# Kernel optimization log

Hardware: AMD Instinct MI355X
Metric: run time of the kernel (lower is better)

## Reference

```python
import jax, jax.numpy as jnp
import numpy as np

N_NODES = 50000
N_EDGES = 800000
IN_CH = 128
HID = 64
HEADS = 4
OUT_CH = 10
NUM_GRAPHS = 500
NEG_SLOPE = 0.2  # PyG GATConv default LeakyReLU slope


def gat_conv(x, src, dst, W, a_src, a_dst, b, concat):
    """One PyG-style GATConv (inference; attention dropout disabled).
    x: [N, F_in], src/dst: [E'] (self-loops already appended).
    W: [F_in, H*C], a_src/a_dst: [H, C], b: [H*C] or [C].
    """
    N = x.shape[0]
    H, C = a_src.shape
    h = (x @ W).reshape(N, H, C)                      # [N,H,C]
    al_s = jnp.einsum('nhc,hc->nh', h, a_src)          # [N,H]
    al_d = jnp.einsum('nhc,hc->nh', h, a_dst)          # [N,H]
    e = al_s[src] + al_d[dst]                          # [E,H]
    e = jnp.where(e > 0, e, NEG_SLOPE * e)             # leaky_relu
    # segment softmax over edges sharing the same destination node
    e_max = jax.ops.segment_max(e, dst, num_segments=N)
    ex = jnp.exp(e - e_max[dst])
    denom = jax.ops.segment_sum(ex, dst, num_segments=N)
    alpha = ex / (denom[dst] + 1e-16)                  # [E,H]
    msg = h[src] * alpha[:, :, None]                   # [E,H,C]
    out = jax.ops.segment_sum(msg, dst, num_segments=N)  # [N,H,C]
    out = out.reshape(N, H * C) if concat else out.mean(axis=1)
    return out + b


def _forward(x, edge_index, batch, W1, a_src1, a_dst1, b1,
             W2, a_src2, a_dst2, b2, fc_w, fc_b):
    N = x.shape[0]
    loops = jnp.arange(N, dtype=edge_index.dtype)
    src = jnp.concatenate([edge_index[0], loops])
    dst = jnp.concatenate([edge_index[1], loops])
    h = gat_conv(x, src, dst, W1, a_src1, a_dst1, b1, concat=True)
    h = jax.nn.relu(h)                                  # dropout: eval mode
    h = gat_conv(h, src, dst, W2, a_src2, a_dst2, b2, concat=False)
    pooled = jax.ops.segment_sum(h, batch, num_segments=NUM_GRAPHS)  # global_add_pool
    logits = pooled @ fc_w + fc_b
    return jax.nn.log_softmax(logits, axis=1)


def setup_inputs() -> dict:
    key = jax.random.key(0)
    ks = jax.random.split(key, 12)
    g = lambda k, shp, fan: jax.random.normal(k, shp, dtype=jnp.float32) * (1.0 / np.sqrt(fan))
    x = jax.random.normal(ks[0], (N_NODES, IN_CH), dtype=jnp.float32)
    edge_index = jax.random.randint(ks[1], (2, N_EDGES), 0, N_NODES, dtype=jnp.int64)
    batch = jnp.sort(jax.random.randint(ks[2], (N_NODES,), 0, NUM_GRAPHS, dtype=jnp.int64))
    return {
        'x': x,
        'edge_index': edge_index,
        'batch': batch,
        'W1': g(ks[3], (IN_CH, HEADS * HID), IN_CH),
        'a_src1': g(ks[4], (HEADS, HID), HID),
        'a_dst1': g(ks[5], (HEADS, HID), HID),
        'b1': jnp.zeros((HEADS * HID,), dtype=jnp.float32),
        'W2': g(ks[6], (HEADS * HID, HID), HEADS * HID),
        'a_src2': g(ks[7], (1, HID), HID),
        'a_dst2': g(ks[8], (1, HID), HID),
        'b2': jnp.zeros((HID,), dtype=jnp.float32),
        'fc_w': g(ks[9], (HID, OUT_CH), HID),
        'fc_b': jnp.zeros((OUT_CH,), dtype=jnp.float32),
    }


def reference(x, edge_index, batch, W1, a_src1, a_dst1, b1,
              W2, a_src2, a_dst2, b2, fc_w, fc_b):
    return _forward(x, edge_index, batch, W1, a_src1, a_dst1, b1,
                    W2, a_src2, a_dst2, b2, fc_w, fc_b)
```

## Files before the change

kernel.cpp:

```cpp
#include <hip/hip_runtime.h>
#include <hip/hip_fp16.h>
#include <math.h>

#define N_NODES   50000
#define N_EDGES   800000
#define IN_CH     128
#define HID       64
#define HEADS     4
#define F1        (HEADS * HID)
#define OUT_CH    10
#define NUM_GRAPHS 500
#define NEG_SLOPE 0.2f
#define RPAD      132
#define NTILES    (N_NODES / 16)
#define CAP       64

typedef __attribute__((ext_vector_type(8))) _Float16 half8;
typedef __attribute__((ext_vector_type(4))) float floatx4;

__device__ __forceinline__ unsigned short f2h(float f) {
    _Float16 h = (_Float16)f;
    unsigned short u; __builtin_memcpy(&u, &h, 2); return u;
}
__device__ __forceinline__ unsigned int pack_h2(float lo, float hi) {
    auto r = __builtin_amdgcn_cvt_pkrtz(lo, hi);
    unsigned int u; __builtin_memcpy(&u, &r, 4); return u;
}
__device__ __forceinline__ float h2f(unsigned short u) {
    _Float16 h; __builtin_memcpy(&h, &u, 2); return (float)h;
}

__global__ void init_kernel(int* __restrict__ cnt, unsigned short* __restrict__ csr,
                            const float* __restrict__ W1, unsigned short* __restrict__ W1p,
                            const float* __restrict__ W2, unsigned short* __restrict__ W2p)
{
    const int gid = blockIdx.x * blockDim.x + threadIdx.x;
    if (gid < N_NODES) {
        cnt[gid] = 1;
        csr[gid * CAP] = (unsigned short)gid;
    }
    if (gid < 4096) {
        const int t = gid >> 8, kt = (gid >> 6) & 3, l = gid & 63;
        const int col = t * 16 + (l & 15);
        unsigned short* o = W1p + (size_t)((t * 4 + kt) * 64 + l) * 8;
        #pragma unroll
        for (int j = 0; j < 8; ++j) {
            const int k = kt * 32 + (l >> 4) * 8 + j;
            o[j] = f2h(W1[k * F1 + col]);
        }
    } else if (gid < 6144) {
        const int g2 = gid - 4096;
        const int t = g2 >> 9, kt = (g2 >> 6) & 7, l = g2 & 63;
        const int col = t * 16 + (l & 15);
        unsigned short* o = W2p + (size_t)((t * 8 + kt) * 64 + l) * 8;
        #pragma unroll
        for (int j = 0; j < 8; ++j) {
            const int k = kt * 32 + (l >> 4) * 8 + j;
            o[j] = f2h(W2[k * HID + col]);
        }
    }
}

__global__ __launch_bounds__(256) void scatter_gemm1(
    const int* __restrict__ ei, int* __restrict__ cnt,
    unsigned short* __restrict__ csr,
    const float* __restrict__ x, const unsigned short* __restrict__ W1p,
    const float* __restrict__ a_src1, const float* __restrict__ a_dst1,
    unsigned short* __restrict__ H1b,
    float* __restrict__ al_s1, float* __restrict__ al_d1)
{
    const int e = blockIdx.x * 256 + threadIdx.x;
    const int src = ei[e];
    const int dst = ei[N_EDGES + e];
    const int slot = atomicAdd(&cnt[dst], 1);

    const int m0 = blockIdx.x * 16;
    const int w = threadIdx.x >> 6;
    const int l = threadIdx.x & 63;
    const int q = l >> 4, r = l & 15;
    floatx4 acc[4] = {};
    const float* arow = x + (size_t)(m0 + r) * IN_CH + q * 8;
    #pragma unroll
    for (int kt = 0; kt < 4; ++kt) {
        const float4 f0 = *(const float4*)(arow + kt * 32);
        const float4 f1 = *(const float4*)(arow + kt * 32 + 4);
        union { uint4 u; half8 h; } a;
        a.u = make_uint4(pack_h2(f0.x, f0.y), pack_h2(f0.z, f0.w),
                         pack_h2(f1.x, f1.y), pack_h2(f1.z, f1.w));
        #pragma unroll
        for (int t = 0; t < 4; ++t) {
            const int nt = w * 4 + t;
            const half8 b = *(const half8*)(W1p + (size_t)((nt * 4 + kt) * 64 + l) * 8);
            acc[t] = __builtin_amdgcn_mfma_f32_16x16x32_f16(a.h, b, acc[t], 0, 0, 0);
        }
    }
    float ls[4] = {0.f, 0.f, 0.f, 0.f}, ld[4] = {0.f, 0.f, 0.f, 0.f};
    #pragma unroll
    for (int t = 0; t < 4; ++t) {
        const int col = (w * 4 + t) * 16 + r;
        const float as = a_src1[col], ad = a_dst1[col];
        #pragma unroll
        for (int reg = 0; reg < 4; ++reg) {
            H1b[(size_t)(m0 + q * 4 + reg) * F1 + col] = f2h(acc[t][reg]);
            ls[reg] += acc[t][reg] * as;
            ld[reg] += acc[t][reg] * ad;
        }
    }
    #pragma unroll
    for (int reg = 0; reg < 4; ++reg) {
        #pragma unroll
        for (int off = 8; off > 0; off >>= 1) {
            ls[reg] += __shfl_down(ls[reg], off, 16);
            ld[reg] += __shfl_down(ld[reg], off, 16);
        }
    }
    if (r == 0) {
        #pragma unroll
        for (int reg = 0; reg < 4; ++reg) {
            const int n = m0 + q * 4 + reg;
            al_s1[n * HEADS + w] = ls[reg];
            al_d1[n * HEADS + w] = ld[reg];
        }
    }

    if (slot < CAP) csr[dst * CAP + slot] = (unsigned short)src;
}

__global__ __launch_bounds__(256) void agg1_gemm2(
    const int* __restrict__ cnt, const unsigned short* __restrict__ csr,
    const float* __restrict__ al_s1, const float* __restrict__ al_d1,
    const uint2* __restrict__ H1b2, const float* __restrict__ b1,
    const unsigned short* __restrict__ W2p,
    const float* __restrict__ a_src2, const float* __restrict__ a_dst2,
    unsigned short* __restrict__ H2b,
    float* __restrict__ al_s2, float* __restrict__ al_d2)
{
    const int m0 = blockIdx.x * 16;
    const int w = threadIdx.x >> 6;
    const int l = threadIdx.x & 63;
    __shared__ unsigned int rows[16][RPAD];
    __shared__ unsigned int sofs[16][CAP];
    __shared__ float        wts[16][CAP][4];

    int nreg[4];
    #pragma unroll
    for (int d = 0; d < 4; ++d) {
        const int dd = w * 4 + d;
        const int dstn = m0 + dd;
        const int n = min(cnt[dstn], CAP);
        nreg[d] = n;
        const float4 ad = *(const float4*)(al_d1 + dstn * 4);
        float w0 = 0.f, w1 = 0.f, w2 = 0.f, w3 = 0.f;
        unsigned int off = 0;
        if (l < n) {
            const int s = csr[dstn * CAP + l];
            off = (unsigned int)s << 9;
            const float4 as = *(const float4*)(al_s1 + s * 4);
            float t0 = as.x + ad.x; t0 = t0 > 0.f ? t0 : NEG_SLOPE * t0;
            float t1 = as.y + ad.y; t1 = t1 > 0.f ? t1 : NEG_SLOPE * t1;
            float t2 = as.z + ad.z; t2 = t2 > 0.f ? t2 : NEG_SLOPE * t2;
            float t3 = as.w + ad.w; t3 = t3 > 0.f ? t3 : NEG_SLOPE * t3;
            w0 = __expf(t0); w1 = __expf(t1); w2 = __expf(t2); w3 = __expf(t3);
        }
        sofs[dd][l] = off;
        *(float4*)wts[dd][l] = make_float4(w0, w1, w2, w3);
    }
    __syncthreads();

    const int h = l >> 4;
    const unsigned int lane8 = (unsigned int)(l * 8);
    #pragma unroll 1
    for (int d = 0; d < 4; ++d) {
        const int dd = w * 4 + d;
        const int n = nreg[d];
        float a0 = 0.f, a1 = 0.f, a2 = 0.f, a3 = 0.f, den = 0.f;
        const int n4 = (n + 3) & ~3;
        for (int i = 0; i < n4; i += 4) {
            unsigned int off[4]; float wt[4];
            #pragma unroll
            for (int j = 0; j < 4; ++j) {
                off[j] = sofs[dd][i + j];
                wt[j]  = wts[dd][i + j][h];
            }
            uint2 u[4];
            #pragma unroll
            for (int j = 0; j < 4; ++j)
                u[j] = *(const uint2*)((const char*)H1b2 + (off[j] + lane8));
            #pragma unroll
            for (int j = 0; j < 4; ++j) {
                union { uint2 v; _Float16 hv[4]; } c; c.v = u[j];
                a0 += wt[j] * (float)c.hv[0];
                a1 += wt[j] * (float)c.hv[1];
                a2 += wt[j] * (float)c.hv[2];
                a3 += wt[j] * (float)c.hv[3];
                den += wt[j];
            }
        }
        const float rcp = 1.f / (den + 1e-16f);
        const float4 bb = *(const float4*)(b1 + 4 * l);
        float v0 = a0 * rcp + bb.x; v0 = v0 > 0.f ? v0 : 0.f;
        float v1 = a1 * rcp + bb.y; v1 = v1 > 0.f ? v1 : 0.f;
        float v2 = a2 * rcp + bb.z; v2 = v2 > 0.f ? v2 : 0.f;
        float v3 = a3 * rcp + bb.w; v3 = v3 > 0.f ? v3 : 0.f;
        *(uint2*)&rows[dd][2 * l] = make_uint2(pack_h2(v0, v1), pack_h2(v2, v3));
    }
    __syncthreads();

    const int q = l >> 4, r = l & 15;
    floatx4 acc = {};
    #pragma unroll
    for (int kt = 0; kt < 8; ++kt) {
        union { uint4 u; half8 hh; } a;
        a.u = *(const uint4*)&rows[r][kt * 16 + q * 4];
        const half8 b = *(const half8*)(W2p + (size_t)((w * 8 + kt) * 64 + l) * 8);
        acc = __builtin_amdgcn_mfma_f32_16x16x32_f16(a.hh, b, acc, 0, 0, 0);
    }
    const int col = w * 16 + r;
    const float as = a_src2[col], ad2 = a_dst2[col];
    float ls[4], ld[4];
    #pragma unroll
    for (int reg = 0; reg < 4; ++reg) {
        H2b[(size_t)(m0 + q * 4 + reg) * HID + col] = f2h(acc[reg]);
        ls[reg] = acc[reg] * as;
        ld[reg] = acc[reg] * ad2;
    }
    #pragma unroll
    for (int reg = 0; reg < 4; ++reg) {
        #pragma unroll
        for (int off = 8; off > 0; off >>= 1) {
            ls[reg] += __shfl_down(ls[reg], off, 16);
            ld[reg] += __shfl_down(ld[reg], off, 16);
        }
    }
    __shared__ float Ls[4][16], Ld[4][16];
    if (r == 0) {
        #pragma unroll
        for (int reg = 0; reg < 4; ++reg) {
            Ls[w][q * 4 + reg] = ls[reg];
            Ld[w][q * 4 + reg] = ld[reg];
        }
    }
    __syncthreads();
    if (threadIdx.x < 16) {
        const int row = threadIdx.x;
        al_s2[m0 + row] = Ls[0][row] + Ls[1][row] + Ls[2][row] + Ls[3][row];
        al_d2[m0 + row] = Ld[0][row] + Ld[1][row] + Ld[2][row] + Ld[3][row];
    }
}

__global__ __launch_bounds__(256) void agg2_csr(
    const int* __restrict__ cnt, const unsigned short* __restrict__ csr,
    const float* __restrict__ al_s2, const float* __restrict__ al_d2,
    const uint2* __restrict__ H2b2, uint2* __restrict__ out2b)
{
    const int dst = blockIdx.x * 4 + (threadIdx.x >> 6);
    const int l = threadIdx.x & 63;
    const int qt = l >> 4, j = l & 15;
    const int n = min(cnt[dst], CAP);
    const float ad = al_d2[dst];
    float a0 = 0.f, a1 = 0.f, a2 = 0.f, a3 = 0.f, den = 0.f;
    int s_reg = 0;
    float w_reg = 0.f;
    if (l < n) {
        s_reg = csr[dst * CAP + l];
        float t = al_s2[s_reg] + ad;
        t = t > 0.f ? t : NEG_SLOPE * t;
        w_reg = __expf(t);
    }
    const int n8 = (n + 7) & ~7;
    for (int i = 0; i < n8; i += 8) {
        const int e0 = i + qt, e1 = i + 4 + qt;
        const int   src0 = __shfl(s_reg, e0, 64), src1 = __shfl(s_reg, e1, 64);
        const float wt0  = __shfl(w_reg, e0, 64), wt1  = __shfl(w_reg, e1, 64);
        const uint2 u0 = H2b2[(size_t)src0 * (HID / 4) + j];
        const uint2 u1 = H2b2[(size_t)src1 * (HID / 4) + j];
        union { uint2 v; _Float16 hv[4]; } c0, c1; c0.v = u0; c1.v = u1;
        a0 += wt0 * (float)c0.hv[0] + wt1 * (float)c1.hv[0];
        a1 += wt0 * (float)c0.hv[1] + wt1 * (float)c1.hv[1];
        a2 += wt0 * (float)c0.hv[2] + wt1 * (float)c1.hv[2];
        a3 += wt0 * (float)c0.hv[3] + wt1 * (float)c1.hv[3];
        den += wt0 + wt1;
    }
    #pragma unroll
    for (int m = 16; m <= 32; m <<= 1) {
        a0 += __shfl_xor(a0, m, 64);
        a1 += __shfl_xor(a1, m, 64);
        a2 += __shfl_xor(a2, m, 64);
        a3 += __shfl_xor(a3, m, 64);
        den += __shfl_xor(den, m, 64);
    }
    if (l < 16) {
        const float rcp = 1.f / (den + 1e-16f);
        out2b[(size_t)dst * (HID / 4) + j] =
            make_uint2(pack_h2(a0 * rcp, a1 * rcp), pack_h2(a2 * rcp, a3 * rcp));
    }
}

__global__ __launch_bounds__(256) void pool_fc_kernel(
    const unsigned short* __restrict__ out2b, const float* __restrict__ b2,
    const int* __restrict__ batch,
    const float* __restrict__ fc_w, const float* __restrict__ fc_b,
    float* __restrict__ out)
{
    const int g = blockIdx.x;
    const int q = threadIdx.x >> 6, c = threadIdx.x & 63;
    __shared__ int se[2];
    __shared__ float partial[4][HID];
    __shared__ float pl[HID];
    __shared__ float logits[OUT_CH];
    if (threadIdx.x < 2) {
        const int target = g + threadIdx.x;
        int lo = 0, hi = N_NODES;
        while (lo < hi) { int mid = (lo + hi) >> 1; if (batch[mid] < target) lo = mid + 1; else hi = mid; }
        se[threadIdx.x] = lo;
    }
    __syncthreads();
    const int start = se[0], end = se[1];
    float acc = 0.f;
    for (int n = start + q; n < end; n += 4)
        acc += h2f(out2b[(size_t)n * HID + c]);
    partial[q][c] = acc;
    __syncthreads();
    if (q == 0)
        pl[c] = partial[0][c] + partial[1][c] + partial[2][c] + partial[3][c]
              + (float)(end - start) * b2[c];
    __syncthreads();
    if (threadIdx.x < OUT_CH) {
        float lg = fc_b[threadIdx.x];
        #pragma unroll
        for (int k = 0; k < HID; ++k) lg += pl[k] * fc_w[k * OUT_CH + threadIdx.x];
        logits[threadIdx.x] = lg;
    }
    __syncthreads();
    if (threadIdx.x == 0) {
        float m = logits[0];
        #pragma unroll
        for (int j2 = 1; j2 < OUT_CH; ++j2) m = fmaxf(m, logits[j2]);
        float s = 0.f;
        #pragma unroll
        for (int j2 = 0; j2 < OUT_CH; ++j2) s += __expf(logits[j2] - m);
        const float lse = m + __logf(s);
        #pragma unroll
        for (int j2 = 0; j2 < OUT_CH; ++j2) out[g * OUT_CH + j2] = logits[j2] - lse;
    }
}


extern "C" void kernel_launch(void* const* d_in, const int* in_sizes, int n_in,
                              void* d_out, int out_size, void* d_ws, size_t ws_size,
                              hipStream_t stream)
{
    const float* x      = (const float*)d_in[0];
    const int*   ei     = (const int*)  d_in[1];
    const int*   batch  = (const int*)  d_in[2];
    const float* W1     = (const float*)d_in[3];
    const float* a_src1 = (const float*)d_in[4];
    const float* a_dst1 = (const float*)d_in[5];
    const float* b1     = (const float*)d_in[6];
    const float* W2     = (const float*)d_in[7];
    const float* a_src2 = (const float*)d_in[8];
    const float* a_dst2 = (const float*)d_in[9];
    const float* b2     = (const float*)d_in[10];
    const float* fc_w   = (const float*)d_in[11];
    const float* fc_b   = (const float*)d_in[12];
    float* out = (float*)d_out;

    char* ws = (char*)d_ws;
    size_t off = 0;
    auto alloc_b = [&](size_t bytes) { void* p = (void*)(ws + off); off += (bytes + 15) & ~15ull; return p; };

    unsigned short* H1b  = (unsigned short*)alloc_b((size_t)N_NODES * F1 * 2);
    float* al_s1  = (float*)alloc_b((size_t)N_NODES * HEADS * 4);
    float* al_d1  = (float*)alloc_b((size_t)N_NODES * HEADS * 4);
    unsigned short* H2b  = (unsigned short*)alloc_b((size_t)N_NODES * HID * 2);
    float* al_s2  = (float*)alloc_b((size_t)N_NODES * 4);
    float* al_d2  = (float*)alloc_b((size_t)N_NODES * 4);
    unsigned short* out2b = (unsigned short*)alloc_b((size_t)N_NODES * HID * 2);
    int*   cnt    = (int*)alloc_b((size_t)N_NODES * 4);
    unsigned short* csr = (unsigned short*)alloc_b((size_t)N_NODES * CAP * 2);
    unsigned short* W1p = (unsigned short*)alloc_b((size_t)IN_CH * F1 * 2);
    unsigned short* W2p = (unsigned short*)alloc_b((size_t)F1 * HID * 2);

    init_kernel<<<(N_NODES + 255) / 256, 256, 0, stream>>>(cnt, csr, W1, W1p, W2, W2p);

    scatter_gemm1<<<NTILES, 256, 0, stream>>>(ei, cnt, csr, x, W1p,
                                              a_src1, a_dst1, H1b, al_s1, al_d1);

    agg1_gemm2<<<N_NODES / 16, 256, 0, stream>>>(cnt, csr, al_s1, al_d1,
                                                 (const uint2*)H1b, b1,
                                                 W2p, a_src2, a_dst2,
                                                 H2b, al_s2, al_d2);

    agg2_csr<<<N_NODES / 4, 256, 0, stream>>>(cnt, csr, al_s2, al_d2,
                                              (const uint2*)H2b, (uint2*)out2b);

    pool_fc_kernel<<<NUM_GRAPHS, 256, 0, stream>>>(out2b, b2, batch, fc_w, fc_b, out);
}
```

Measured before the change: 240.0 us.

## Store layer-1 features as FP8 e4m3 and gather 16 channels per lane

The layer-1 hidden features H1 are now stored as FP8 e4m3 instead of FP16, which halves the bytes moved by the random-access neighbor gather in agg1_gemm2. The gather is reorganized so each lane loads 16 FP8 channels (uint4) and the four 16-lane groups each process different edges, followed by cross-group shuffle reductions. Attention weights are packed into FP16 in shared memory. The risks are accuracy loss from 8-bit feature storage, extra conversion ALU work and more registers per thread.

Result: no change. 243.0 us (+1.2%).

```diff
diff --git a/kernel.cpp b/kernel.cpp
--- a/kernel.cpp
+++ b/kernel.cpp
@@ -1,5 +1,6 @@
 #include <hip/hip_runtime.h>
 #include <hip/hip_fp16.h>
+#include <hip/hip_fp8.h>
 #include <math.h>
 
 #define N_NODES   50000
@@ -29,6 +30,13 @@
 __device__ __forceinline__ float h2f(unsigned short u) {
     _Float16 h; __builtin_memcpy(&h, &u, 2); return (float)h;
 }
+__device__ __forceinline__ unsigned char f2q(float f) {
+    __hip_fp8_e4m3 q(f);
+    unsigned char u; __builtin_memcpy(&u, &q, 1); return u;
+}
+__device__ __forceinline__ float q2f(unsigned char u) {
+    __hip_fp8_e4m3 q; __builtin_memcpy(&q, &u, 1); return (float)q;
+}
 
 __global__ void init_kernel(int* __restrict__ cnt, unsigned short* __restrict__ csr,
                             const float* __restrict__ W1, unsigned short* __restrict__ W1p,
@@ -66,7 +74,7 @@
     unsigned short* __restrict__ csr,
     const float* __restrict__ x, const unsigned short* __restrict__ W1p,
     const float* __restrict__ a_src1, const float* __restrict__ a_dst1,
-    unsigned short* __restrict__ H1b,
+    unsigned char* __restrict__ H1q,
     float* __restrict__ al_s1, float* __restrict__ al_d1)
 {
     const int e = blockIdx.x * 256 + threadIdx.x;
@@ -101,7 +109,7 @@
         const float as = a_src1[col], ad = a_dst1[col];
         #pragma unroll
         for (int reg = 0; reg < 4; ++reg) {
-            H1b[(size_t)(m0 + q * 4 + reg) * F1 + col] = f2h(acc[t][reg]);
+            H1q[(size_t)(m0 + q * 4 + reg) * F1 + col] = f2q(acc[t][reg]);
             ls[reg] += acc[t][reg] * as;
             ld[reg] += acc[t][reg] * ad;
         }
@@ -129,7 +137,7 @@
 __global__ __launch_bounds__(256) void agg1_gemm2(
     const int* __restrict__ cnt, const unsigned short* __restrict__ csr,
     const float* __restrict__ al_s1, const float* __restrict__ al_d1,
-    const uint2* __restrict__ H1b2, const float* __restrict__ b1,
+    const unsigned char* __restrict__ H1q, const float* __restrict__ b1,
     const unsigned short* __restrict__ W2p,
     const float* __restrict__ a_src2, const float* __restrict__ a_dst2,
     unsigned short* __restrict__ H2b,
@@ -138,9 +146,10 @@
     const int m0 = blockIdx.x * 16;
     const int w = threadIdx.x >> 6;
     const int l = threadIdx.x & 63;
+    const char* H1base = (const char*)H1q;
     __shared__ unsigned int rows[16][RPAD];
     __shared__ unsigned int sofs[16][CAP];
-    __shared__ float        wts[16][CAP][4];
+    __shared__ uint2        wtp[16][CAP];
 
     int nreg[4];
     #pragma unroll
@@ -154,7 +163,7 @@
         unsigned int off = 0;
         if (l < n) {
             const int s = csr[dstn * CAP + l];
-            off = (unsigned int)s << 9;
+            off = (unsigned int)s << 8;
             const float4 as = *(const float4*)(al_s1 + s * 4);
             float t0 = as.x + ad.x; t0 = t0 > 0.f ? t0 : NEG_SLOPE * t0;
             float t1 = as.y + ad.y; t1 = t1 > 0.f ? t1 : NEG_SLOPE * t1;
@@ -163,46 +172,64 @@
             w0 = __expf(t0); w1 = __expf(t1); w2 = __expf(t2); w3 = __expf(t3);
         }
         sofs[dd][l] = off;
-        *(float4*)wts[dd][l] = make_float4(w0, w1, w2, w3);
-    }
-    __syncthreads();
-
-    const int h = l >> 4;
-    const unsigned int lane8 = (unsigned int)(l * 8);
+        wtp[dd][l] = make_uint2(pack_h2(w0, w1), pack_h2(w2, w3));
+    }
+    __syncthreads();
+
+    const int qe = l >> 4;
+    const int j  = l & 15;
+    const int hd = j >> 2;
+    const unsigned int lane16 = (unsigned int)(j * 16);
     #pragma unroll 1
     for (int d = 0; d < 4; ++d) {
         const int dd = w * 4 + d;
         const int n = nreg[d];
-        float a0 = 0.f, a1 = 0.f, a2 = 0.f, a3 = 0.f, den = 0.f;
-        const int n4 = (n + 3) & ~3;
-        for (int i = 0; i < n4; i += 4) {
+        float A[16] = {};
+        float den = 0.f;
+        const int n16 = (n + 15) & ~15;
+        for (int i = 0; i < n16; i += 16) {
             unsigned int off[4]; float wt[4];
             #pragma unroll
-            for (int j = 0; j < 4; ++j) {
-                off[j] = sofs[dd][i + j];
-                wt[j]  = wts[dd][i + j][h];
+            for (int k = 0; k < 4; ++k) {
+                const int slot = i + 4 * k + qe;
+                off[k] = sofs[dd][slot];
+                const uint2 wp = wtp[dd][slot];
+                const unsigned int uw = (hd & 2) ? wp.y : wp.x;
+                wt[k] = h2f((hd & 1) ? (unsigned short)(uw >> 16)
+                                     : (unsigned short)(uw & 0xFFFFu));
             }
-            uint2 u[4];
+            uint4 u[4];
             #pragma unroll
-            for (int j = 0; j < 4; ++j)
-                u[j] = *(const uint2*)((const char*)H1b2 + (off[j] + lane8));
+            for (int k = 0; k < 4; ++k)
+                u[k] = *(const uint4*)(H1base + (off[k] + lane16));
             #pragma unroll
-            for (int j = 0; j < 4; ++j) {
-                union { uint2 v; _Float16 hv[4]; } c; c.v = u[j];
-                a0 += wt[j] * (float)c.hv[0];
-                a1 += wt[j] * (float)c.hv[1];
-                a2 += wt[j] * (float)c.hv[2];
-                a3 += wt[j] * (float)c.hv[3];
-                den += wt[j];
+            for (int k = 0; k < 4; ++k) {
+                union { uint4 v; unsigned char b[16]; } c; c.v = u[k];
+                #pragma unroll
+                for (int ch = 0; ch < 16; ++ch)
+                    A[ch] += wt[k] * q2f(c.b[ch]);
+                den += wt[k];
             }
         }
-        const float rcp = 1.f / (den + 1e-16f);
-        const float4 bb = *(const float4*)(b1 + 4 * l);
-        float v0 = a0 * rcp + bb.x; v0 = v0 > 0.f ? v0 : 0.f;
-        float v1 = a1 * rcp + bb.y; v1 = v1 > 0.f ? v1 : 0.f;
-        float v2 = a2 * rcp + bb.z; v2 = v2 > 0.f ? v2 : 0.f;
-        float v3 = a3 * rcp + bb.w; v3 = v3 > 0.f ? v3 : 0.f;
-        *(uint2*)&rows[dd][2 * l] = make_uint2(pack_h2(v0, v1), pack_h2(v2, v3));
+        #pragma unroll
+        for (int ch = 0; ch < 16; ++ch) {
+            A[ch] += __shfl_xor(A[ch], 16, 64);
+            A[ch] += __shfl_xor(A[ch], 32, 64);
+        }
+        den += __shfl_xor(den, 16, 64);
+        den += __shfl_xor(den, 32, 64);
+        if (l < 16) {
+            const float rcp = 1.f / (den + 1e-16f);
+            unsigned int o[8];
+            #pragma unroll
+            for (int p = 0; p < 8; ++p) {
+                const float va = fmaxf(A[2 * p]     * rcp + b1[16 * j + 2 * p],     0.f);
+                const float vb = fmaxf(A[2 * p + 1] * rcp + b1[16 * j + 2 * p + 1], 0.f);
+                o[p] = pack_h2(va, vb);
+            }
+            *(uint4*)&rows[dd][8 * j]     = make_uint4(o[0], o[1], o[2], o[3]);
+            *(uint4*)&rows[dd][8 * j + 4] = make_uint4(o[4], o[5], o[6], o[7]);
+        }
     }
     __syncthreads();
 
@@ -210,10 +237,10 @@
     floatx4 acc = {};
     #pragma unroll
     for (int kt = 0; kt < 8; ++kt) {
-        union { uint4 u; half8 hh; } a;
+        union { uint4 u; half8 hh2; } a;
         a.u = *(const uint4*)&rows[r][kt * 16 + q * 4];
         const half8 b = *(const half8*)(W2p + (size_t)((w * 8 + kt) * 64 + l) * 8);
-        acc = __builtin_amdgcn_mfma_f32_16x16x32_f16(a.hh, b, acc, 0, 0, 0);
+        acc = __builtin_amdgcn_mfma_f32_16x16x32_f16(a.hh2, b, acc, 0, 0, 0);
     }
     const int col = w * 16 + r;
     const float as = a_src2[col], ad2 = a_dst2[col];
@@ -369,7 +396,7 @@
     size_t off = 0;
     auto alloc_b = [&](size_t bytes) { void* p = (void*)(ws + off); off += (bytes + 15) & ~15ull; return p; };
 
-    unsigned short* H1b  = (unsigned short*)alloc_b((size_t)N_NODES * F1 * 2);
+    unsigned char*  H1q  = (unsigned char*)alloc_b((size_t)N_NODES * F1);
     float* al_s1  = (float*)alloc_b((size_t)N_NODES * HEADS * 4);
     float* al_d1  = (float*)alloc_b((size_t)N_NODES * HEADS * 4);
     unsigned short* H2b  = (unsigned short*)alloc_b((size_t)N_NODES * HID * 2);
@@ -384,10 +411,10 @@
     init_kernel<<<(N_NODES + 255) / 256, 256, 0, stream>>>(cnt, csr, W1, W1p, W2, W2p);
 
     scatter_gemm1<<<NTILES, 256, 0, stream>>>(ei, cnt, csr, x, W1p,
-                                              a_src1, a_dst1, H1b, al_s1, al_d1);
+                                              a_src1, a_dst1, H1q, al_s1, al_d1);
 
     agg1_gemm2<<<N_NODES / 16, 256, 0, stream>>>(cnt, csr, al_s1, al_d1,
-                                                 (const uint2*)H1b, b1,
+                                                 H1q, b1,
                                                  W2p, a_src2, a_dst2,
                                                  H2b, al_s2, al_d2);
 
```
